# Kernel tuning notes

Measured on AMD Instinct MI355X. Metric: run time of the kernel, lower is better.

The kernel has to match this reference:

```python
import jax, jax.numpy as jnp
import numpy as np

B, L = 4096, 200
N_USERS, N_ITEMS, N_CATS, N_DUR = 200000, 500000, 1000, 20
D = 64  # item_embed_dim == seq_embed_dim


def _lin(k, din, dout):
    kw, kb = jax.random.split(k)
    s = 1.0 / np.sqrt(din)
    return (jax.random.uniform(kw, (din, dout), minval=-s, maxval=s),
            jax.random.uniform(kb, (dout,), minval=-s, maxval=s))


def setup_inputs() -> dict:
    key = jax.random.key(0)
    ks = jax.random.split(key, 20)
    inp = {
        'user_id': jax.random.randint(ks[0], (B,), 0, N_USERS),
        'item_id': jax.random.randint(ks[1], (B,), 0, N_ITEMS),
        'item_category': jax.random.randint(ks[2], (B,), 0, N_CATS),
        'item_dur_bkt': jax.random.randint(ks[3], (B,), 0, N_DUR),
        'user_dense': jax.random.normal(ks[4], (B, 25), dtype=jnp.float32),
        'item_dense': jax.random.normal(ks[5], (B, 3), dtype=jnp.float32),
        'history_seq': jax.random.randint(ks[6], (B, L), 0, N_ITEMS + 1),
        # embedding tables (init std=0.01 as in _init_weights)
        'user_W': 0.01 * jax.random.normal(ks[7], (N_USERS, 64), dtype=jnp.float32),
        'item_W': 0.01 * jax.random.normal(ks[8], (N_ITEMS, D), dtype=jnp.float32),
        'cat_W': 0.01 * jax.random.normal(ks[9], (N_CATS, 16), dtype=jnp.float32),
        'dur_W': 0.01 * jax.random.normal(ks[10], (N_DUR, 8), dtype=jnp.float32),
        'hist_W': 0.01 * jax.random.normal(ks[11], (N_ITEMS + 1, D), dtype=jnp.float32),
    }
    # attention MLP: 4*D=256 -> 64 -> 32 -> 1
    inp['aW0'], inp['ab0'] = _lin(ks[12], 4 * D, 64)
    inp['aW1'], inp['ab1'] = _lin(ks[13], 64, 32)
    inp['aW2'], inp['ab2'] = _lin(ks[14], 32, 1)
    # final MLP: concat_dim 64+64+16+8+25+3+64 = 244 -> 256 -> 128 -> 1
    inp['mW0'], inp['mb0'] = _lin(ks[15], 244, 256)
    inp['mW1'], inp['mb1'] = _lin(ks[16], 256, 128)
    inp['mW2'], inp['mb2'] = _lin(ks[17], 128, 1)
    return inp


def reference(user_id, item_id, item_category, item_dur_bkt, user_dense, item_dense,
              history_seq, user_W, item_W, cat_W, dur_W, hist_W,
              aW0, ab0, aW1, ab1, aW2, ab2, mW0, mb0, mW1, mb1, mW2, mb2):
    u_emb = user_W[user_id]            # (B, 64)
    i_emb = item_W[item_id]            # (B, D)
    c_emb = cat_W[item_category]       # (B, 16)
    d_emb = dur_W[item_dur_bkt]        # (B, 8)
    hist = hist_W[history_seq]         # (B, L, D)

    t = i_emb[:, None, :]              # (B, 1, D); item_dim == seq_dim so no slice
    tb = jnp.broadcast_to(t, hist.shape)
    feat = jnp.concatenate([hist, tb, hist * t, hist - t], axis=-1)  # (B, L, 4D)

    h = jax.nn.relu(feat @ aW0 + ab0)
    h = jax.nn.relu(h @ aW1 + ab1)
    scores = (h @ aW2 + ab2)[..., 0]   # (B, L)

    pad_mask = history_seq == 0
    scores = jnp.where(pad_mask, jnp.float32(-1e9), scores)
    w = jax.nn.softmax(scores, axis=-1)                # (B, L)
    pooled = jnp.einsum('bl,bld->bd', w, hist)         # (B, D)

    x = jnp.concatenate([u_emb, i_emb, c_emb, d_emb, user_dense, item_dense, pooled], axis=-1)
    h = jax.nn.relu(x @ mW0 + mb0)     # dropout is identity in eval mode
    h = jax.nn.relu(h @ mW1 + mb1)
    logit = (h @ mW2 + mb2)[..., 0]
    return jax.nn.sigmoid(logit)       # (B,)
```

## Files before the change

### kernel.cpp

```cpp
#include <hip/hip_runtime.h>

#define L_SZ 200
#define RB 8
#define HS_STRIDE 72

typedef __attribute__((ext_vector_type(8))) short short8;
typedef __attribute__((ext_vector_type(4))) float floatx4;

__device__ __forceinline__ unsigned short f2bf(float f) {
    unsigned int u = __float_as_uint(f);
    unsigned int r = (u + 0x7fffu + ((u >> 16) & 1u)) >> 16;
    return (unsigned short)r;
}
__device__ __forceinline__ float bf2f(unsigned short h) {
    return __uint_as_float(((unsigned int)h) << 16);
}
__device__ __forceinline__ unsigned int pk2(float a, float b) {
    unsigned int r;
    asm("v_cvt_pk_bf16_f32 %0, %1, %2" : "=v"(r) : "v"(a), "v"(b));
    return r;
}
__device__ __forceinline__ float wave_sum64(float v) {
    #pragma unroll
    for (int m = 1; m <= 32; m <<= 1) v += __shfl_xor(v, m, 64);
    return v;
}
__device__ __forceinline__ float wave_max64(float v) {
    #pragma unroll
    for (int m = 1; m <= 32; m <<= 1) v = fmaxf(v, __shfl_xor(v, m, 64));
    return v;
}
__device__ __forceinline__ void bar_lds() {
    asm volatile("s_waitcnt lgkmcnt(0)" ::: "memory");
    __builtin_amdgcn_s_barrier();
    asm volatile("" ::: "memory");
}

__global__ __launch_bounds__(256) void prep_kernel(
    const int* __restrict__ item_id, const float* __restrict__ item_W,
    const float* __restrict__ aW0, const float* __restrict__ ab0,
    const float* __restrict__ aW1,
    float* __restrict__ T1t, float* __restrict__ T2t,
    unsigned short* __restrict__ PW1, float* __restrict__ cb_ws)
{
    __shared__ float shbuf[3 * 64 * 65];
    const int tid = threadIdx.x;
    if (blockIdx.x == 0) {
        #pragma unroll
        for (int t = 0; t < 3; ++t) {
            const int r0 = (t == 0) ? 0 : (t == 1) ? 128 : 192;
            for (int u = tid; u < 1024; u += 256) {
                int k = u >> 4, c4 = u & 15;
                float4 v = *(const float4*)(aW0 + (r0 + k) * 64 + c4 * 4);
                float* dst = shbuf + t * 4160 + k * 65 + c4 * 4;
                dst[0] = v.x; dst[1] = v.y; dst[2] = v.z; dst[3] = v.w;
            }
        }
        __syncthreads();
        for (int u = tid; u < 4096; u += 256) {
            int j = u >> 6, k = u & 63;
            T1t[u] = shbuf[k * 65 + j] + shbuf[2 * 4160 + k * 65 + j];
            T2t[u] = shbuf[4160 + k * 65 + j];
        }
        for (int u = tid; u < 2048; u += 256) {
            int i = u & 7, lane = (u >> 3) & 63, f = u >> 9;
            int nt = f >> 1, ks = f & 1;
            int k = ks * 32 + (lane >> 4) * 8 + i;
            int n = nt * 16 + (lane & 15);
            PW1[u] = f2bf(aW1[k * 32 + n]);
        }
    } else {
        float* T3 = shbuf;
        float* IE = shbuf + 64 * 65;
        const int B0 = (blockIdx.x - 1) * 64;
        for (int u = tid; u < 4096; u += 256) {
            int k = u >> 6, j = u & 63;
            T3[k * 65 + j] = aW0[(64 + k) * 64 + j] - aW0[(192 + k) * 64 + j];
        }
        for (int u = tid; u < 4096; u += 256) {
            int r = u >> 6, j = u & 63;
            IE[r * 64 + j] = item_W[(size_t)item_id[B0 + r] * 64 + j];
        }
        __syncthreads();
        const int j = tid & 63, rg = tid >> 6;
        for (int pass = 0; pass < 16; ++pass) {
            int bl = rg * 16 + pass;
            float acc = ab0[j];
            #pragma unroll 8
            for (int k = 0; k < 64; ++k)
                acc = fmaf(IE[bl * 64 + k], T3[k * 65 + j], acc);
            cb_ws[(size_t)(B0 + bl) * 64 + j] = acc;
        }
    }
}

__global__ __launch_bounds__(256, 4) void attn_kernel(
    const int* __restrict__ item_id, const int* __restrict__ hist_seq,
    const float* __restrict__ item_W, const float* __restrict__ hist_W,
    const float* __restrict__ T1t, const float* __restrict__ T2t,
    const unsigned short* __restrict__ PW1, const float* __restrict__ cb_ws,
    const float* __restrict__ ab1, const float* __restrict__ aW2,
    const float* __restrict__ ab2, float* __restrict__ pooled_ws)
{
    __shared__ __align__(16) unsigned char smem[38624];
    unsigned short* Hs  = (unsigned short*)(smem);
    unsigned short* BB  = (unsigned short*)(smem + 28800);
    int*   seq_sh = (int*)(smem + 36992);
    float* scores = (float*)(smem + 37792);
    float* red    = (float*)(smem + 38592);

    const int tid  = threadIdx.x;
    const int w    = tid >> 6;
    const int lane = tid & 63;
    const int b    = blockIdx.x;
    const int* hseq = hist_seq + b * L_SZ;

    if (tid < L_SZ) seq_sh[tid] = hseq[tid];

    const int rbase = tid >> 3, c8 = tid & 7;
    const bool extra = tid < 64;
    const int r6 = extra ? 192 + rbase : 0;
    const float* sp[7];
    #pragma unroll
    for (int t = 0; t < 6; ++t)
        sp[t] = hist_W + (size_t)hseq[rbase + t * 32] * 64 + c8 * 8;
    sp[6] = hist_W + (size_t)hseq[r6] * 64 + c8 * 8;
    float4 f0[7], f1[7];
    #pragma unroll
    for (int t = 0; t < 7; ++t) {
        f0[t] = *(const float4*)sp[t];
        f1[t] = *(const float4*)(sp[t] + 4);
    }

    const int c = lane & 15, q = lane >> 4;
    short8 bW1[2][2];
    #pragma unroll
    for (int nt = 0; nt < 2; ++nt)
        #pragma unroll
        for (int ks = 0; ks < 2; ++ks)
            bW1[nt][ks] = *(const short8*)(PW1 + ((nt * 2 + ks) * 64 + lane) * 8);
    float cbr[4];
    #pragma unroll
    for (int nt = 0; nt < 4; ++nt) cbr[nt] = cb_ws[(size_t)b * 64 + nt * 16 + c];
    float ab1r[2], aw2r[2];
    #pragma unroll
    for (int nt = 0; nt < 2; ++nt) {
        ab1r[nt] = ab1[nt * 16 + c];
        aw2r[nt] = aW2[nt * 16 + c];
    }
    const float ab2s = ab2[0];

    #pragma unroll
    for (int t = 0; t < 6; ++t) {
        uint4 pk;
        pk.x = pk2(f0[t].x, f0[t].y); pk.y = pk2(f0[t].z, f0[t].w);
        pk.z = pk2(f1[t].x, f1[t].y); pk.w = pk2(f1[t].z, f1[t].w);
        *(uint4*)(Hs + (rbase + t * 32) * HS_STRIDE + c8 * 8) = pk;
    }
    if (extra) {
        uint4 pk;
        pk.x = pk2(f0[6].x, f0[6].y); pk.y = pk2(f0[6].z, f0[6].w);
        pk.z = pk2(f1[6].x, f1[6].y); pk.w = pk2(f1[6].z, f1[6].w);
        *(uint4*)(Hs + r6 * HS_STRIDE + c8 * 8) = pk;
    }

    {
        const float* irow = item_W + (size_t)item_id[b] * 64;
        const int j0 = tid >> 3;
        float4 em0 = *(const float4*)(irow + c8 * 8);
        float4 em1 = *(const float4*)(irow + c8 * 8 + 4);
        #pragma unroll
        for (int t = 0; t < 2; ++t) {
            int j = j0 + t * 32;
            const float* p1 = T1t + j * 64 + c8 * 8;
            const float* p2 = T2t + j * 64 + c8 * 8;
            float4 a0 = *(const float4*)p1, a1 = *(const float4*)(p1 + 4);
            float4 b0 = *(const float4*)p2, b1 = *(const float4*)(p2 + 4);
            float v[8];
            v[0] = a0.x + em0.x * b0.x; v[1] = a0.y + em0.y * b0.y;
            v[2] = a0.z + em0.z * b0.z; v[3] = a0.w + em0.w * b0.w;
            v[4] = a1.x + em1.x * b1.x; v[5] = a1.y + em1.y * b1.y;
            v[6] = a1.z + em1.z * b1.z; v[7] = a1.w + em1.w * b1.w;
            uint4 pk;
            pk.x = pk2(v[0], v[1]); pk.y = pk2(v[2], v[3]);
            pk.z = pk2(v[4], v[5]); pk.w = pk2(v[6], v[7]);
            *(uint4*)(BB + j * 64 + (c8 ^ (j & 7)) * 8) = pk;
        }
    }
    bar_lds();

    short8 bW[4][2];
    #pragma unroll
    for (int nt = 0; nt < 4; ++nt)
        #pragma unroll
        for (int ks = 0; ks < 2; ++ks)
            bW[nt][ks] = *(const short8*)(BB + (nt * 16 + c) * 64
                                             + ((4 * ks + q) ^ (c & 7)) * 8);
    bar_lds();

    unsigned short* scrw = BB + w * (16 * 64);
    const floatx4 zf = {0.f, 0.f, 0.f, 0.f};

    for (int mt = w; mt < 13; mt += 4) {
        const int rowbase = mt * 16;
        floatx4 acc0[4] = {zf, zf, zf, zf};
        #pragma unroll
        for (int ks = 0; ks < 2; ++ks) {
            short8 a = *(const short8*)(Hs + (rowbase + c) * HS_STRIDE + ks * 32 + q * 8);
            acc0[0] = __builtin_amdgcn_mfma_f32_16x16x32_bf16(a, bW[0][ks], acc0[0], 0, 0, 0);
            acc0[1] = __builtin_amdgcn_mfma_f32_16x16x32_bf16(a, bW[1][ks], acc0[1], 0, 0, 0);
            acc0[2] = __builtin_amdgcn_mfma_f32_16x16x32_bf16(a, bW[2][ks], acc0[2], 0, 0, 0);
            acc0[3] = __builtin_amdgcn_mfma_f32_16x16x32_bf16(a, bW[3][ks], acc0[3], 0, 0, 0);
        }
        #pragma unroll
        for (int nt = 0; nt < 4; ++nt)
            #pragma unroll
            for (int r = 0; r < 4; r += 2) {
                float h0 = fmaxf(acc0[nt][r]     + cbr[nt], 0.f);
                float h1 = fmaxf(acc0[nt][r + 1] + cbr[nt], 0.f);
                unsigned int u = pk2(h0, h1);
                int row0 = q * 4 + r;
                int row1 = row0 + 1;
                int gp0 = (2 * nt + (c >> 3)) ^ (row0 & 7);
                int gp1 = (2 * nt + (c >> 3)) ^ (row1 & 7);
                scrw[row0 * 64 + gp0 * 8 + (c & 7)] = (unsigned short)u;
                scrw[row1 * 64 + gp1 * 8 + (c & 7)] = (unsigned short)(u >> 16);
            }
        floatx4 acc1[2] = {zf, zf};
        #pragma unroll
        for (int ks = 0; ks < 2; ++ks) {
            short8 a1 = *(const short8*)(scrw + c * 64 + ((4 * ks + q) ^ (c & 7)) * 8);
            acc1[0] = __builtin_amdgcn_mfma_f32_16x16x32_bf16(a1, bW1[0][ks], acc1[0], 0, 0, 0);
            acc1[1] = __builtin_amdgcn_mfma_f32_16x16x32_bf16(a1, bW1[1][ks], acc1[1], 0, 0, 0);
        }
        float s[4];
        #pragma unroll
        for (int r = 0; r < 4; ++r)
            s[r] = fmaxf(acc1[0][r] + ab1r[0], 0.f) * aw2r[0]
                 + fmaxf(acc1[1][r] + ab1r[1], 0.f) * aw2r[1];
        #pragma unroll
        for (int m = 1; m <= 8; m <<= 1)
            #pragma unroll
            for (int r = 0; r < 4; ++r) s[r] += __shfl_xor(s[r], m, 64);
        if (c == 0) {
            #pragma unroll
            for (int r = 0; r < 4; ++r) {
                int l = rowbase + q * 4 + r;
                if (l < L_SZ)
                    scores[l] = (seq_sh[l] == 0) ? -1.0e9f : (s[r] + ab2s);
            }
        }
    }
    bar_lds();

    float s0 = (tid < L_SZ) ? scores[tid] : -3.0e38f;
    float mx = wave_max64(s0);
    if (lane == 0) red[w] = mx;
    bar_lds();
    mx = fmaxf(fmaxf(red[0], red[1]), fmaxf(red[2], red[3]));
    float e = (tid < L_SZ) ? __expf(s0 - mx) : 0.f;
    float sm = wave_sum64(e);
    if (lane == 0) red[4 + w] = sm;
    bar_lds();
    const float winv = 1.f / ((red[4] + red[5]) + (red[6] + red[7]));
    if (tid < L_SZ) scores[tid] = e * winv;
    bar_lds();

    float* pools = (float*)BB;
    {
        int g  = (w << 1) | (lane >> 5);
        int jj = lane & 31;
        int l0 = g * 26, l1 = (l0 + 26 < L_SZ) ? l0 + 26 : L_SZ;
        float p0 = 0.f, p1 = 0.f;
        for (int l = l0; l < l1; ++l) {
            float wt = scores[l];
            unsigned int pv = *(const unsigned int*)(Hs + l * HS_STRIDE + jj * 2);
            p0 = fmaf(wt, bf2f((unsigned short)(pv & 0xffffu)), p0);
            p1 = fmaf(wt, bf2f((unsigned short)(pv >> 16)), p1);
        }
        float2 pp = {p0, p1};
        *(float2*)&pools[g * 64 + jj * 2] = pp;
    }
    bar_lds();
    if (tid < 64) {
        float sum = 0.f;
        #pragma unroll
        for (int g = 0; g < 8; ++g) sum += pools[g * 64 + tid];
        pooled_ws[(size_t)b * 64 + tid] = sum;
    }
}

__global__ __launch_bounds__(256) void mlp_kernel(
    const int* __restrict__ user_id, const int* __restrict__ item_id,
    const int* __restrict__ item_cat, const int* __restrict__ item_dur,
    const float* __restrict__ user_dense, const float* __restrict__ item_dense,
    const float* __restrict__ user_W, const float* __restrict__ item_W,
    const float* __restrict__ cat_W, const float* __restrict__ dur_W,
    const float* __restrict__ mW0, const float* __restrict__ mb0,
    const float* __restrict__ mW1, const float* __restrict__ mb1,
    const float* __restrict__ mW2, const float* __restrict__ mb2,
    const float* __restrict__ pooled_ws, float* __restrict__ out)
{
    __shared__ __align__(16) float xT[244][RB];
    __shared__ __align__(16) float h0T[256][RB];
    __shared__ __align__(16) float h1T[128][RB];
    __shared__ __align__(16) float part[128][RB];

    const int tid = threadIdx.x;
    const int b0 = blockIdx.x * RB;

    for (int idx = tid; idx < 244 * RB; idx += 256) {
        int r = idx / 244;
        int c = idx - r * 244;
        int b = b0 + r;
        float v;
        if (c < 64)       v = user_W[(size_t)user_id[b] * 64 + c];
        else if (c < 128) v = item_W[(size_t)item_id[b] * 64 + (c - 64)];
        else if (c < 144) v = cat_W[item_cat[b] * 16 + (c - 128)];
        else if (c < 152) v = dur_W[item_dur[b] * 8 + (c - 144)];
        else if (c < 177) v = user_dense[b * 25 + (c - 152)];
        else if (c < 180) v = item_dense[b * 3 + (c - 177)];
        else              v = pooled_ws[(size_t)b * 64 + (c - 180)];
        xT[c][r] = v;
    }
    __syncthreads();

    {
        float acc[RB];
        const float bias = mb0[tid];
        #pragma unroll
        for (int r = 0; r < RB; ++r) acc[r] = bias;
        #pragma unroll 4
        for (int k = 0; k < 244; ++k) {
            float wk = mW0[k * 256 + tid];
            float4 xa = *(const float4*)&xT[k][0];
            float4 xb = *(const float4*)&xT[k][4];
            acc[0] = fmaf(wk, xa.x, acc[0]);
            acc[1] = fmaf(wk, xa.y, acc[1]);
            acc[2] = fmaf(wk, xa.z, acc[2]);
            acc[3] = fmaf(wk, xa.w, acc[3]);
            acc[4] = fmaf(wk, xb.x, acc[4]);
            acc[5] = fmaf(wk, xb.y, acc[5]);
            acc[6] = fmaf(wk, xb.z, acc[6]);
            acc[7] = fmaf(wk, xb.w, acc[7]);
        }
        #pragma unroll
        for (int r = 0; r < RB; ++r) h0T[tid][r] = fmaxf(acc[r], 0.f);
    }
    __syncthreads();

    const int jj = tid & 127;
    const int half = tid >> 7;
    {
        float acc[RB];
        #pragma unroll
        for (int r = 0; r < RB; ++r) acc[r] = 0.f;
        #pragma unroll 4
        for (int t = 0; t < 128; ++t) {
            int k = half * 128 + t;
            float wk = mW1[k * 128 + jj];
            float4 ha = *(const float4*)&h0T[k][0];
            float4 hb = *(const float4*)&h0T[k][4];
            acc[0] = fmaf(wk, ha.x, acc[0]);
            acc[1] = fmaf(wk, ha.y, acc[1]);
            acc[2] = fmaf(wk, ha.z, acc[2]);
            acc[3] = fmaf(wk, ha.w, acc[3]);
            acc[4] = fmaf(wk, hb.x, acc[4]);
            acc[5] = fmaf(wk, hb.y, acc[5]);
            acc[6] = fmaf(wk, hb.z, acc[6]);
            acc[7] = fmaf(wk, hb.w, acc[7]);
        }
        if (half == 1) {
            #pragma unroll
            for (int r = 0; r < RB; ++r) part[jj][r] = acc[r];
        }
        __syncthreads();
        if (half == 0) {
            const float bias = mb1[jj];
            #pragma unroll
            for (int r = 0; r < RB; ++r)
                h1T[jj][r] = fmaxf(acc[r] + part[jj][r] + bias, 0.f);
        }
    }
    __syncthreads();

    if (tid < RB) {
        const int r = tid;
        float a0 = mb2[0], a1 = 0.f;
        #pragma unroll 8
        for (int k = 0; k < 128; k += 2) {
            a0 = fmaf(h1T[k][r],     mW2[k],     a0);
            a1 = fmaf(h1T[k + 1][r], mW2[k + 1], a1);
        }
        float a = a0 + a1;
        out[b0 + r] = 1.f / (1.f + __expf(-a));
    }
}

extern "C" void kernel_launch(void* const* d_in, const int* in_sizes, int n_in,
                              void* d_out, int out_size, void* d_ws, size_t ws_size,
                              hipStream_t stream) {
    (void)in_sizes; (void)n_in; (void)out_size; (void)ws_size;
    const int*   user_id    = (const int*)d_in[0];
    const int*   item_id    = (const int*)d_in[1];
    const int*   item_cat   = (const int*)d_in[2];
    const int*   item_dur   = (const int*)d_in[3];
    const float* user_dense = (const float*)d_in[4];
    const float* item_dense = (const float*)d_in[5];
    const int*   hist_seq   = (const int*)d_in[6];
    const float* user_W     = (const float*)d_in[7];
    const float* item_W     = (const float*)d_in[8];
    const float* cat_W      = (const float*)d_in[9];
    const float* dur_W      = (const float*)d_in[10];
    const float* hist_W     = (const float*)d_in[11];
    const float* aW0 = (const float*)d_in[12];
    const float* ab0 = (const float*)d_in[13];
    const float* aW1 = (const float*)d_in[14];
    const float* ab1 = (const float*)d_in[15];
    const float* aW2 = (const float*)d_in[16];
    const float* ab2 = (const float*)d_in[17];
    const float* mW0 = (const float*)d_in[18];
    const float* mb0 = (const float*)d_in[19];
    const float* mW1 = (const float*)d_in[20];
    const float* mb1 = (const float*)d_in[21];
    const float* mW2 = (const float*)d_in[22];
    const float* mb2 = (const float*)d_in[23];
    float* out = (float*)d_out;

    char* ws = (char*)d_ws;
    float* pooled_ws = (float*)ws;
    float* cb_ws     = (float*)(ws + (1u << 20));
    float* T1t       = (float*)(ws + (2u << 20));
    float* T2t       = (float*)(ws + (2u << 20) + 16384);
    unsigned short* PW1 = (unsigned short*)(ws + (2u << 20) + 32768);

    prep_kernel<<<65, 256, 0, stream>>>(item_id, item_W, aW0, ab0, aW1,
                                        T1t, T2t, PW1, cb_ws);
    attn_kernel<<<4096, 256, 0, stream>>>(item_id, hist_seq, item_W, hist_W,
                                          T1t, T2t, PW1, cb_ws,
                                          ab1, aW2, ab2, pooled_ws);
    mlp_kernel<<<4096 / RB, 256, 0, stream>>>(user_id, item_id, item_cat, item_dur,
                                              user_dense, item_dense,
                                              user_W, item_W, cat_W, dur_W,
                                              mW0, mb0, mW1, mb1, mW2, mb2,
                                              pooled_ws, out);
}
```

Measured before the change: 398.7 us.

## Fold prep kernel into attention kernel, computing folded weights per block

Removes the separate prep kernel launch. Each attention block now builds its per-item folded layer-0 weight matrix and bias vector on the fly from aW0, ab0 and aW1, using shuffle reductions and a small LDS buffer. This drops one launch and its serialization on the stream. In exchange, every one of the 4096 blocks rereads all of aW0 (64KB, mostly served from L2) and does extra ALU work and scattered 2-byte LDS stores.

```diff
diff --git a/kernel.cpp b/kernel.cpp
--- a/kernel.cpp
+++ b/kernel.cpp
@@ -7,11 +7,6 @@
 typedef __attribute__((ext_vector_type(8))) short short8;
 typedef __attribute__((ext_vector_type(4))) float floatx4;
 
-__device__ __forceinline__ unsigned short f2bf(float f) {
-    unsigned int u = __float_as_uint(f);
-    unsigned int r = (u + 0x7fffu + ((u >> 16) & 1u)) >> 16;
-    return (unsigned short)r;
-}
 __device__ __forceinline__ float bf2f(unsigned short h) {
     return __uint_as_float(((unsigned int)h) << 16);
 }
@@ -20,6 +15,9 @@
     asm("v_cvt_pk_bf16_f32 %0, %1, %2" : "=v"(r) : "v"(a), "v"(b));
     return r;
 }
+__device__ __forceinline__ unsigned short bf1(float a) {
+    return (unsigned short)(pk2(a, a) & 0xffffu);
+}
 __device__ __forceinline__ float wave_sum64(float v) {
     #pragma unroll
     for (int m = 1; m <= 32; m <<= 1) v += __shfl_xor(v, m, 64);
@@ -36,78 +34,21 @@
     asm volatile("" ::: "memory");
 }
 
-__global__ __launch_bounds__(256) void prep_kernel(
-    const int* __restrict__ item_id, const float* __restrict__ item_W,
-    const float* __restrict__ aW0, const float* __restrict__ ab0,
-    const float* __restrict__ aW1,
-    float* __restrict__ T1t, float* __restrict__ T2t,
-    unsigned short* __restrict__ PW1, float* __restrict__ cb_ws)
-{
-    __shared__ float shbuf[3 * 64 * 65];
-    const int tid = threadIdx.x;
-    if (blockIdx.x == 0) {
-        #pragma unroll
-        for (int t = 0; t < 3; ++t) {
-            const int r0 = (t == 0) ? 0 : (t == 1) ? 128 : 192;
-            for (int u = tid; u < 1024; u += 256) {
-                int k = u >> 4, c4 = u & 15;
-                float4 v = *(const float4*)(aW0 + (r0 + k) * 64 + c4 * 4);
-                float* dst = shbuf + t * 4160 + k * 65 + c4 * 4;
-                dst[0] = v.x; dst[1] = v.y; dst[2] = v.z; dst[3] = v.w;
-            }
-        }
-        __syncthreads();
-        for (int u = tid; u < 4096; u += 256) {
-            int j = u >> 6, k = u & 63;
-            T1t[u] = shbuf[k * 65 + j] + shbuf[2 * 4160 + k * 65 + j];
-            T2t[u] = shbuf[4160 + k * 65 + j];
-        }
-        for (int u = tid; u < 2048; u += 256) {
-            int i = u & 7, lane = (u >> 3) & 63, f = u >> 9;
-            int nt = f >> 1, ks = f & 1;
-            int k = ks * 32 + (lane >> 4) * 8 + i;
-            int n = nt * 16 + (lane & 15);
-            PW1[u] = f2bf(aW1[k * 32 + n]);
-        }
-    } else {
-        float* T3 = shbuf;
-        float* IE = shbuf + 64 * 65;
-        const int B0 = (blockIdx.x - 1) * 64;
-        for (int u = tid; u < 4096; u += 256) {
-            int k = u >> 6, j = u & 63;
-            T3[k * 65 + j] = aW0[(64 + k) * 64 + j] - aW0[(192 + k) * 64 + j];
-        }
-        for (int u = tid; u < 4096; u += 256) {
-            int r = u >> 6, j = u & 63;
-            IE[r * 64 + j] = item_W[(size_t)item_id[B0 + r] * 64 + j];
-        }
-        __syncthreads();
-        const int j = tid & 63, rg = tid >> 6;
-        for (int pass = 0; pass < 16; ++pass) {
-            int bl = rg * 16 + pass;
-            float acc = ab0[j];
-            #pragma unroll 8
-            for (int k = 0; k < 64; ++k)
-                acc = fmaf(IE[bl * 64 + k], T3[k * 65 + j], acc);
-            cb_ws[(size_t)(B0 + bl) * 64 + j] = acc;
-        }
-    }
-}
-
 __global__ __launch_bounds__(256, 4) void attn_kernel(
     const int* __restrict__ item_id, const int* __restrict__ hist_seq,
     const float* __restrict__ item_W, const float* __restrict__ hist_W,
-    const float* __restrict__ T1t, const float* __restrict__ T2t,
-    const unsigned short* __restrict__ PW1, const float* __restrict__ cb_ws,
-    const float* __restrict__ ab1, const float* __restrict__ aW2,
-    const float* __restrict__ ab2, float* __restrict__ pooled_ws)
+    const float* __restrict__ aW0, const float* __restrict__ ab0,
+    const float* __restrict__ aW1, const float* __restrict__ ab1,
+    const float* __restrict__ aW2, const float* __restrict__ ab2,
+    float* __restrict__ pooled_ws)
 {
-    __shared__ __align__(16) unsigned char smem[38624];
+    __shared__ __align__(16) unsigned char smem[39648];
     unsigned short* Hs  = (unsigned short*)(smem);
     unsigned short* BB  = (unsigned short*)(smem + 28800);
     int*   seq_sh = (int*)(smem + 36992);
     float* scores = (float*)(smem + 37792);
     float* red    = (float*)(smem + 38592);
+    float* cbp    = (float*)(smem + 38624);
 
     const int tid  = threadIdx.x;
     const int w    = tid >> 6;
@@ -137,11 +78,20 @@
     #pragma unroll
     for (int nt = 0; nt < 2; ++nt)
         #pragma unroll
-        for (int ks = 0; ks < 2; ++ks)
-            bW1[nt][ks] = *(const short8*)(PW1 + ((nt * 2 + ks) * 64 + lane) * 8);
-    float cbr[4];
-    #pragma unroll
-    for (int nt = 0; nt < 4; ++nt) cbr[nt] = cb_ws[(size_t)b * 64 + nt * 16 + c];
+        for (int ks = 0; ks < 2; ++ks) {
+            float v[8];
+            #pragma unroll
+            for (int i = 0; i < 8; ++i)
+                v[i] = aW1[(ks * 32 + q * 8 + i) * 32 + nt * 16 + c];
+            uint4 uu;
+            uu.x = pk2(v[0], v[1]); uu.y = pk2(v[2], v[3]);
+            uu.z = pk2(v[4], v[5]); uu.w = pk2(v[6], v[7]);
+            short8 r; *(uint4*)&r = uu;
+            bW1[nt][ks] = r;
+        }
+    float ab0r[4];
+    #pragma unroll
+    for (int nt = 0; nt < 4; ++nt) ab0r[nt] = ab0[nt * 16 + c];
     float ab1r[2], aw2r[2];
     #pragma unroll
     for (int nt = 0; nt < 2; ++nt) {
@@ -165,26 +115,47 @@
     }
 
     {
-        const float* irow = item_W + (size_t)item_id[b] * 64;
-        const int j0 = tid >> 3;
-        float4 em0 = *(const float4*)(irow + c8 * 8);
-        float4 em1 = *(const float4*)(irow + c8 * 8 + 4);
-        #pragma unroll
-        for (int t = 0; t < 2; ++t) {
-            int j = j0 + t * 32;
-            const float* p1 = T1t + j * 64 + c8 * 8;
-            const float* p2 = T2t + j * 64 + c8 * 8;
-            float4 a0 = *(const float4*)p1, a1 = *(const float4*)(p1 + 4);
-            float4 b0 = *(const float4*)p2, b1 = *(const float4*)(p2 + 4);
-            float v[8];
-            v[0] = a0.x + em0.x * b0.x; v[1] = a0.y + em0.y * b0.y;
-            v[2] = a0.z + em0.z * b0.z; v[3] = a0.w + em0.w * b0.w;
-            v[4] = a1.x + em1.x * b1.x; v[5] = a1.y + em1.y * b1.y;
-            v[6] = a1.z + em1.z * b1.z; v[7] = a1.w + em1.w * b1.w;
-            uint4 pk;
-            pk.x = pk2(v[0], v[1]); pk.y = pk2(v[2], v[3]);
-            pk.z = pk2(v[4], v[5]); pk.w = pk2(v[6], v[7]);
-            *(uint4*)(BB + j * 64 + (c8 ^ (j & 7)) * 8) = pk;
+        const int kk = tid >> 2;
+        const int jq = tid & 3;
+        const float ie_k = item_W[(size_t)item_id[b] * 64 + kk];
+        const float4* a0p = (const float4*)(aW0 + kk * 64 + jq * 16);
+        const float4* a1p = (const float4*)(aW0 + (64 + kk) * 64 + jq * 16);
+        const float4* a2p = (const float4*)(aW0 + (128 + kk) * 64 + jq * 16);
+        const float4* a3p = (const float4*)(aW0 + (192 + kk) * 64 + jq * 16);
+        float4 A0[4], A1[4], A2[4], A3[4];
+        #pragma unroll
+        for (int t = 0; t < 4; ++t) {
+            A0[t] = a0p[t]; A1[t] = a1p[t]; A2[t] = a2p[t]; A3[t] = a3p[t];
+        }
+        const int k8g = kk >> 3, k7 = kk & 7;
+        float cbv[16];
+        #pragma unroll
+        for (int t = 0; t < 4; ++t) {
+            const float* p0 = (const float*)&A0[t];
+            const float* p1 = (const float*)&A1[t];
+            const float* p2 = (const float*)&A2[t];
+            const float* p3 = (const float*)&A3[t];
+            #pragma unroll
+            for (int u = 0; u < 4; ++u) {
+                int j = jq * 16 + t * 4 + u;
+                float we = p0[u] + p3[u] + ie_k * p2[u];
+                BB[j * 64 + ((k8g ^ (j & 7)) << 3) + k7] = bf1(we);
+                cbv[t * 4 + u] = ie_k * (p1[u] - p3[u]);
+            }
+        }
+        #pragma unroll
+        for (int t = 0; t < 16; ++t) {
+            float p = cbv[t];
+            p += __shfl_xor(p, 4, 64);
+            p += __shfl_xor(p, 8, 64);
+            p += __shfl_xor(p, 16, 64);
+            p += __shfl_xor(p, 32, 64);
+            cbv[t] = p;
+        }
+        if ((lane >> 2) == 0) {
+            #pragma unroll
+            for (int t = 0; t < 16; ++t)
+                cbp[w * 64 + jq * 16 + t] = cbv[t];
         }
     }
     bar_lds();
@@ -196,6 +167,12 @@
         for (int ks = 0; ks < 2; ++ks)
             bW[nt][ks] = *(const short8*)(BB + (nt * 16 + c) * 64
                                              + ((4 * ks + q) ^ (c & 7)) * 8);
+    float cbr[4];
+    #pragma unroll
+    for (int nt = 0; nt < 4; ++nt) {
+        int j = nt * 16 + c;
+        cbr[nt] = ab0r[nt] + ((cbp[j] + cbp[64 + j]) + (cbp[128 + j] + cbp[192 + j]));
+    }
     bar_lds();
 
     unsigned short* scrw = BB + w * (16 * 64);
@@ -426,19 +403,11 @@
     const float* mW2 = (const float*)d_in[22];
     const float* mb2 = (const float*)d_in[23];
     float* out = (float*)d_out;
-
-    char* ws = (char*)d_ws;
-    float* pooled_ws = (float*)ws;
-    float* cb_ws     = (float*)(ws + (1u << 20));
-    float* T1t       = (float*)(ws + (2u << 20));
-    float* T2t       = (float*)(ws + (2u << 20) + 16384);
-    unsigned short* PW1 = (unsigned short*)(ws + (2u << 20) + 32768);
-
-    prep_kernel<<<65, 256, 0, stream>>>(item_id, item_W, aW0, ab0, aW1,
-                                        T1t, T2t, PW1, cb_ws);
+    float* pooled_ws = (float*)d_ws;
+
     attn_kernel<<<4096, 256, 0, stream>>>(item_id, hist_seq, item_W, hist_W,
-                                          T1t, T2t, PW1, cb_ws,
-                                          ab1, aW2, ab2, pooled_ws);
+                                          aW0, ab0, aW1, ab1, aW2, ab2,
+                                          pooled_ws);
     mlp_kernel<<<4096 / RB, 256, 0, stream>>>(user_id, item_id, item_cat, item_dur,
                                               user_dense, item_dense,
                                               user_W, item_W, cat_W, dur_W,
```

New measurement: 393.9 us. Within noise of the previous version (-1.2%).
